# Optimization experiments

Measured on AMD Instinct MI355X. Metric: run time of the kernel, lower is better.

The kernel has to match this reference:

```python
import jax, jax.numpy as jnp
import numpy as np

A0 = 0.5291772105638411
KE = 14.399645351950548


def _softplus_inverse(x):
    return x + np.log(-np.expm1(-x))


def _sigma(x):
    # exp(-1/clamp(x,1e-12)) underflows to 0 for x<=0, so the where is nan-free
    return jnp.where(x > 0, jnp.exp(-1.0 / jnp.maximum(x, 1e-12)), 0.0)


def _switch(x, x_on, x_off):
    c = (x - x_on) / (x_off - x_on)
    s1 = _sigma(1.0 - c)
    s0 = _sigma(c)
    return s1 / (s1 + s0 + 1e-12)


def setup_inputs() -> dict:
    key = jax.random.key(0)
    k0, k1, k2, k3, k4 = jax.random.split(key, 5)
    N = 100000
    E = 6400000
    atomic_numbers = jax.random.uniform(k0, (N,), jnp.float32, 1.0, 30.0)
    cutoffs = jax.random.uniform(k1, (E, 1), jnp.float32)
    lengths = jax.random.uniform(k2, (E, 1), jnp.float32, 0.5, 3.0)
    senders = jax.random.randint(k3, (E,), 0, N)
    receivers = jax.random.randint(k4, (E,), 0, N)
    init = dict(a1=3.2, a2=0.9423, a3=0.4028, a4=0.2016,
                c1=0.1818, c2=0.5099, c3=0.2802, c4=0.02817,
                p=0.23, d=1.0 / (0.8854 * A0))
    params = {k + '_raw': jnp.asarray([_softplus_inverse(v)], jnp.float32)
              for k, v in init.items()}
    out = {'atomic_numbers': atomic_numbers, 'cutoffs': cutoffs,
           'senders': senders, 'receivers': receivers,
           'lengths': lengths, 'num_nodes': N}
    out.update(params)
    return out


def reference(atomic_numbers, cutoffs, senders, receivers, lengths, num_nodes,
              a1_raw, a2_raw, a3_raw, a4_raw,
              c1_raw, c2_raw, c3_raw, c4_raw, p_raw, d_raw):
    sp = jax.nn.softplus
    a1, a2, a3, a4 = sp(a1_raw), sp(a2_raw), sp(a3_raw), sp(a4_raw)
    c1, c2, c3, c4 = sp(c1_raw), sp(c2_raw), sp(c3_raw), sp(c4_raw)
    p, d = sp(p_raw), sp(d_raw)
    c_sum = c1 + c2 + c3 + c4
    c1, c2, c3, c4 = c1 / c_sum, c2 / c_sum, c3 / c_sum, c4 / c_sum

    cut = cutoffs[:, 0]   # [E]
    L = lengths[:, 0]     # [E]
    z_i = atomic_numbers[receivers]
    z_j = atomic_numbers[senders]

    x = KE * cut * (z_i * z_j) / jnp.maximum(L, 1e-6)
    rzd = L * (jnp.power(z_i, p) + jnp.power(z_j, p)) * d
    y = (c1 * jnp.exp(-a1 * rzd) + c2 * jnp.exp(-a2 * rzd)
         + c3 * jnp.exp(-a3 * rzd) + c4 * jnp.exp(-a4 * rzd))
    w = _switch(L, 0.0, 1.5)
    e_rep_edge = w * x * y * 0.5
    return jax.ops.segment_sum(e_rep_edge, receivers, num_segments=num_nodes)[:, None]
```

## Files before the change

kernel.cpp:

```cpp
#include <hip/hip_runtime.h>
#include <math.h>

#define C0KE 7.199822675975274f
#define LOG2E 1.4426950408889634f
#define BSHIFT 8
#define NB 391
#define NBP 392
#define K1B 512
#define K1T 1024
#define PLCAP 12512

__device__ __forceinline__ float softplusf(float x) {
    return (x > 20.0f) ? x : log1pf(__expf(x));
}

struct ZblParams { float A1, A2, A3, A4, c1, c2, c3, c4, p; };

__device__ __forceinline__ void load_params(
    const float* a1r, const float* a2r, const float* a3r, const float* a4r,
    const float* c1r, const float* c2r, const float* c3r, const float* c4r,
    const float* pr, const float* dr, ZblParams* P)
{
    float d  = softplusf(dr[0]);
    float s  = d * LOG2E;
    P->A1 = softplusf(a1r[0]) * s;
    P->A2 = softplusf(a2r[0]) * s;
    P->A3 = softplusf(a3r[0]) * s;
    P->A4 = softplusf(a4r[0]) * s;
    float c1 = softplusf(c1r[0]), c2 = softplusf(c2r[0]);
    float c3 = softplusf(c3r[0]), c4 = softplusf(c4r[0]);
    float inv = 1.0f / (c1 + c2 + c3 + c4);
    P->c1 = c1 * inv; P->c2 = c2 * inv; P->c3 = c3 * inv; P->c4 = c4 * inv;
    P->p = softplusf(pr[0]);
}

__device__ __forceinline__ float edge_energy_fast(
    float l, float cut_, float zi, float zj, const ZblParams& P)
{
    float c  = l * (1.0f / 1.5f);
    float om = 1.0f - c;
    float s1 = __builtin_amdgcn_exp2f(-LOG2E * __builtin_amdgcn_rcpf(om));
    float s0 = __builtin_amdgcn_exp2f(-LOG2E * __builtin_amdgcn_rcpf(c));
    float w  = s1 * __builtin_amdgcn_rcpf(s1 + s0);
    float x  = C0KE * cut_ * zi * zj * __builtin_amdgcn_rcpf(l);
    float S  = __builtin_amdgcn_exp2f(P.p * __builtin_amdgcn_logf(zi))
             + __builtin_amdgcn_exp2f(P.p * __builtin_amdgcn_logf(zj));
    float t  = l * S;
    float y  = P.c1 * __builtin_amdgcn_exp2f(-P.A1 * t)
             + P.c2 * __builtin_amdgcn_exp2f(-P.A2 * t)
             + P.c3 * __builtin_amdgcn_exp2f(-P.A3 * t)
             + P.c4 * __builtin_amdgcn_exp2f(-P.A4 * t);
    return w * x * y;
}

__global__ __launch_bounds__(K1T) void zbl_build(
    const float* __restrict__ z, const float* __restrict__ cut,
    const int* __restrict__ snd, const int* __restrict__ rcv,
    const float* __restrict__ len,
    const float* __restrict__ a1r, const float* __restrict__ a2r,
    const float* __restrict__ a3r, const float* __restrict__ a4r,
    const float* __restrict__ c1r, const float* __restrict__ c2r,
    const float* __restrict__ c3r, const float* __restrict__ c4r,
    const float* __restrict__ pr,  const float* __restrict__ dr,
    unsigned* __restrict__ T,
    unsigned* __restrict__ Pg,
    int RSTRIDE, int EPB, int E)
{
    __shared__ ZblParams P;
    __shared__ unsigned chist[NB];
    __shared__ unsigned cbase[NBP];
    __shared__ unsigned fillc[NB];
    __shared__ unsigned wavesum[16];
    __shared__ unsigned pl[PLCAP];

    const int tid = threadIdx.x;
    if (tid == 0)
        load_params(a1r, a2r, a3r, a4r, c1r, c2r, c3r, c4r, pr, dr, &P);
    for (int b = tid; b < NB; b += K1T) { chist[b] = 0u; fillc[b] = 0u; }
    __syncthreads();
    const ZblParams Pl = P;

    const int blk = blockIdx.x;
    const int e0 = blk * EPB;
    const int e1 = min(e0 + EPB, E);
    const int nv = (e1 > e0) ? ((e1 - e0) >> 2) : 0;
    const int qb = e0 >> 2;
    const int etail = e0 + (nv << 2);

    for (int q = tid; q < nv; q += K1T) {
        float4 l4 = ((const float4*)len)[qb + q];
        int4   r4 = ((const int4*)rcv)[qb + q];
        if (l4.x < 1.5f) atomicAdd(&chist[((unsigned)r4.x) >> BSHIFT], 1u);
        if (l4.y < 1.5f) atomicAdd(&chist[((unsigned)r4.y) >> BSHIFT], 1u);
        if (l4.z < 1.5f) atomicAdd(&chist[((unsigned)r4.z) >> BSHIFT], 1u);
        if (l4.w < 1.5f) atomicAdd(&chist[((unsigned)r4.w) >> BSHIFT], 1u);
    }
    for (int e = etail + tid; e < e1; e += K1T)
        if (len[e] < 1.5f) atomicAdd(&chist[((unsigned)rcv[e]) >> BSHIFT], 1u);
    __syncthreads();

    {
        const int lane = tid & 63, wv = tid >> 6;
        unsigned own = (tid < NB) ? chist[tid] : 0u;
        unsigned v = own;
        #pragma unroll
        for (int o = 1; o < 64; o <<= 1) {
            unsigned u = __shfl_up(v, o);
            if (lane >= o) v += u;
        }
        if (lane == 63 && wv < 7) wavesum[wv] = v;
        __syncthreads();
        if (wv == 0) {
            unsigned s = (lane < 7) ? wavesum[lane] : 0u;
            #pragma unroll
            for (int o = 1; o < 8; o <<= 1) {
                unsigned u = __shfl_up(s, o);
                if (lane >= o) s += u;
            }
            if (lane < 7) wavesum[lane] = s;
        }
        __syncthreads();
        unsigned off = (wv > 0 && wv < 8) ? wavesum[wv - 1] : 0u;
        if (tid < NB) cbase[tid] = off + v - own;
        if (tid == 0) cbase[NB] = wavesum[6];
    }
    __syncthreads();

    const unsigned blkbase = (unsigned)blk * (unsigned)RSTRIDE;
    const unsigned trow = (unsigned)blk * (unsigned)NBP;
    for (int b = tid; b <= NB; b += K1T)
        T[trow + b] = blkbase + cbase[b];

    for (int q = tid; q < nv; q += K1T) {
        float4 l4 = ((const float4*)len)[qb + q];
        if (l4.x < 1.5f || l4.y < 1.5f || l4.z < 1.5f || l4.w < 1.5f) {
            float4 c4 = ((const float4*)cut)[qb + q];
            int4   s4 = ((const int4*)snd)[qb + q];
            int4   r4 = ((const int4*)rcv)[qb + q];
            float Ls[4] = {l4.x, l4.y, l4.z, l4.w};
            float Cs[4] = {c4.x, c4.y, c4.z, c4.w};
            int   Ss[4] = {s4.x, s4.y, s4.z, s4.w};
            int   Rs[4] = {r4.x, r4.y, r4.z, r4.w};
            #pragma unroll
            for (int k = 0; k < 4; ++k) {
                if (Ls[k] < 1.5f) {
                    unsigned r = (unsigned)Rs[k];
                    float v = edge_energy_fast(Ls[k], Cs[k],
                                               z[r], z[(unsigned)Ss[k]], Pl);
                    unsigned bk = r >> BSHIFT;
                    unsigned tk = atomicAdd(&fillc[bk], 1u);
                    pl[cbase[bk] + tk] = (__float_as_uint(v) & 0xFFFFFF00u)
                                       | (r & 0xFFu);
                }
            }
        }
    }
    for (int e = etail + tid; e < e1; e += K1T) {
        float l = len[e];
        if (l < 1.5f) {
            unsigned r = (unsigned)rcv[e];
            float v = edge_energy_fast(l, cut[e], z[r], z[(unsigned)snd[e]], Pl);
            unsigned bk = r >> BSHIFT;
            unsigned tk = atomicAdd(&fillc[bk], 1u);
            pl[cbase[bk] + tk] = (__float_as_uint(v) & 0xFFFFFF00u) | (r & 0xFFu);
        }
    }
    __syncthreads();

    const unsigned csum = cbase[NB];
    for (unsigned s = tid; s < csum; s += K1T)
        Pg[blkbase + s] = pl[s];
}

__global__ __launch_bounds__(512) void zbl_reduce(
    const unsigned* __restrict__ T, const unsigned* __restrict__ Pg,
    float* __restrict__ out, int N)
{
    __shared__ float acc[256];
    const int tid = threadIdx.x;
    if (tid < 256) acc[tid] = 0.0f;
    __syncthreads();

    const int b = blockIdx.x;
    for (int r = tid; r < K1B; r += 512) {
        const unsigned* row = T + (size_t)r * NBP;
        unsigned s = row[b];
        unsigned e = row[b + 1];
        for (unsigned i = s; i < e; ++i) {
            unsigned p = Pg[i];
            atomicAdd(&acc[p & 255u], __uint_as_float(p & 0xFFFFFF00u));
        }
    }
    __syncthreads();

    int n = (b << BSHIFT) + tid;
    if (tid < 256 && n < N) out[n] = acc[tid];
}

__global__ __launch_bounds__(256) void zbl_direct(
    const float* __restrict__ z, const float* __restrict__ cut,
    const int* __restrict__ snd, const int* __restrict__ rcv,
    const float* __restrict__ len,
    const float* __restrict__ a1r, const float* __restrict__ a2r,
    const float* __restrict__ a3r, const float* __restrict__ a4r,
    const float* __restrict__ c1r, const float* __restrict__ c2r,
    const float* __restrict__ c3r, const float* __restrict__ c4r,
    const float* __restrict__ pr,  const float* __restrict__ dr,
    float* __restrict__ out, int n4, int E)
{
    __shared__ ZblParams P;
    if (threadIdx.x == 0)
        load_params(a1r, a2r, a3r, a4r, c1r, c2r, c3r, c4r, pr, dr, &P);
    __syncthreads();
    const ZblParams Pl = P;

    int i = blockIdx.x * blockDim.x + threadIdx.x;
    if (i >= n4) return;
    int base = i * 4;
    float cs[4], Ls[4]; int ss[4], rr[4]; int cnt;
    if (base + 4 <= E) {
        float4 c4v = ((const float4*)cut)[i];
        float4 l4v = ((const float4*)len)[i];
        int4   s4v = ((const int4*)snd)[i];
        int4   r4v = ((const int4*)rcv)[i];
        cs[0]=c4v.x; cs[1]=c4v.y; cs[2]=c4v.z; cs[3]=c4v.w;
        Ls[0]=l4v.x; Ls[1]=l4v.y; Ls[2]=l4v.z; Ls[3]=l4v.w;
        ss[0]=s4v.x; ss[1]=s4v.y; ss[2]=s4v.z; ss[3]=s4v.w;
        rr[0]=r4v.x; rr[1]=r4v.y; rr[2]=r4v.z; rr[3]=r4v.w;
        cnt = 4;
    } else {
        cnt = E - base;
        for (int k = 0; k < cnt; ++k) {
            cs[k] = cut[base+k]; Ls[k] = len[base+k];
            ss[k] = snd[base+k]; rr[k] = rcv[base+k];
        }
    }
    #pragma unroll
    for (int k = 0; k < 4; ++k) {
        if (k >= cnt) break;
        if (Ls[k] < 1.5f) {
            float e_rep = edge_energy_fast(Ls[k], cs[k], z[rr[k]], z[ss[k]], Pl);
            unsafeAtomicAdd(&out[rr[k]], e_rep);
        }
    }
}

extern "C" void kernel_launch(void* const* d_in, const int* in_sizes, int n_in,
                              void* d_out, int out_size, void* d_ws, size_t ws_size,
                              hipStream_t stream) {
    const float* z   = (const float*)d_in[0];
    const float* cut = (const float*)d_in[1];
    const int*   snd = (const int*)d_in[2];
    const int*   rcv = (const int*)d_in[3];
    const float* len = (const float*)d_in[4];
    const float* a1r = (const float*)d_in[6];
    const float* a2r = (const float*)d_in[7];
    const float* a3r = (const float*)d_in[8];
    const float* a4r = (const float*)d_in[9];
    const float* c1r = (const float*)d_in[10];
    const float* c2r = (const float*)d_in[11];
    const float* c3r = (const float*)d_in[12];
    const float* c4r = (const float*)d_in[13];
    const float* pr  = (const float*)d_in[14];
    const float* dr  = (const float*)d_in[15];

    float* out = (float*)d_out;
    int E = in_sizes[2];
    int N = out_size;

    int EPB = (((E + K1B - 1) / K1B) + 3) & ~3;
    int RSTRIDE = (EPB + 15) & ~15;
    size_t tsz = ((size_t)K1B * NBP * sizeof(unsigned) + 255) & ~(size_t)255;
    size_t need1 = tsz + (size_t)K1B * RSTRIDE * sizeof(unsigned);

    if (EPB <= PLCAP && ws_size >= need1) {
        unsigned* T  = (unsigned*)d_ws;
        unsigned* Pg = (unsigned*)((char*)d_ws + tsz);
        hipLaunchKernelGGL(zbl_build, dim3(K1B), dim3(K1T), 0, stream,
                           z, cut, snd, rcv, len,
                           a1r, a2r, a3r, a4r, c1r, c2r, c3r, c4r, pr, dr,
                           T, Pg, RSTRIDE, EPB, E);
        hipLaunchKernelGGL(zbl_reduce, dim3(NB), dim3(512), 0, stream,
                           (const unsigned*)T, (const unsigned*)Pg, out, N);
    } else {
        hipMemsetAsync(d_out, 0, (size_t)N * sizeof(float), stream);
        int n4 = (E + 3) / 4;
        int blocks = (n4 + 255) / 256;
        hipLaunchKernelGGL(zbl_direct, dim3(blocks), dim3(256), 0, stream,
                           z, cut, snd, rcv, len,
                           a1r, a2r, a3r, a4r, c1r, c2r, c3r, c4r, pr, dr,
                           out, n4, E);
    }
}
```

Baseline: 207.3 us.

## Replace counting-sort bucketing with fixed-slot per-bucket staging plus global-atomic overflow

The build kernel drops the histogram pass and prefix scan. Each block now writes edges into fixed 16-slot regions per receiver bucket in shared memory, and any overflow goes to global atomics on the output, which is zeroed by a memset first. The reduce kernel reads fixed-stride uint4 slot regions, skips sentinel entries, and adds its sums into the output. This removes a second pass over the len/rcv arrays, the scan and the offset table. The cost is more blocks with 512 threads, a larger padded staging buffer, and possible global atomic contention when a bucket exceeds its slots.

```diff
diff --git a/kernel.cpp b/kernel.cpp
--- a/kernel.cpp
+++ b/kernel.cpp
@@ -4,11 +4,12 @@
 #define C0KE 7.199822675975274f
 #define LOG2E 1.4426950408889634f
 #define BSHIFT 8
-#define NB 391
-#define NBP 392
-#define K1B 512
-#define K1T 1024
-#define PLCAP 12512
+#define NBK 391
+#define SLOTS 16
+#define REG (NBK * SLOTS)
+#define NBLK 1024
+#define K1T 512
+#define SENTINEL 0xFFFFFFFFu
 
 __device__ __forceinline__ float softplusf(float x) {
     return (x > 20.0f) ? x : log1pf(__expf(x));
@@ -62,21 +63,19 @@
     const float* __restrict__ c1r, const float* __restrict__ c2r,
     const float* __restrict__ c3r, const float* __restrict__ c4r,
     const float* __restrict__ pr,  const float* __restrict__ dr,
-    unsigned* __restrict__ T,
     unsigned* __restrict__ Pg,
-    int RSTRIDE, int EPB, int E)
+    float* __restrict__ out,
+    int EPB, int E)
 {
     __shared__ ZblParams P;
-    __shared__ unsigned chist[NB];
-    __shared__ unsigned cbase[NBP];
-    __shared__ unsigned fillc[NB];
-    __shared__ unsigned wavesum[16];
-    __shared__ unsigned pl[PLCAP];
+    __shared__ unsigned slots[REG];
+    __shared__ unsigned fillc[NBK];
 
     const int tid = threadIdx.x;
     if (tid == 0)
         load_params(a1r, a2r, a3r, a4r, c1r, c2r, c3r, c4r, pr, dr, &P);
-    for (int b = tid; b < NB; b += K1T) { chist[b] = 0u; fillc[b] = 0u; }
+    for (int i = tid; i < REG; i += K1T) slots[i] = SENTINEL;
+    for (int b = tid; b < NBK; b += K1T) fillc[b] = 0u;
     __syncthreads();
     const ZblParams Pl = P;
 
@@ -86,57 +85,17 @@
     const int nv = (e1 > e0) ? ((e1 - e0) >> 2) : 0;
     const int qb = e0 >> 2;
     const int etail = e0 + (nv << 2);
+    const float4* Lq = (const float4*)len;
+    const int4*   Rq = (const int4*)rcv;
+    const float4* Cq = (const float4*)cut;
+    const int4*   Sq = (const int4*)snd;
 
     for (int q = tid; q < nv; q += K1T) {
-        float4 l4 = ((const float4*)len)[qb + q];
-        int4   r4 = ((const int4*)rcv)[qb + q];
-        if (l4.x < 1.5f) atomicAdd(&chist[((unsigned)r4.x) >> BSHIFT], 1u);
-        if (l4.y < 1.5f) atomicAdd(&chist[((unsigned)r4.y) >> BSHIFT], 1u);
-        if (l4.z < 1.5f) atomicAdd(&chist[((unsigned)r4.z) >> BSHIFT], 1u);
-        if (l4.w < 1.5f) atomicAdd(&chist[((unsigned)r4.w) >> BSHIFT], 1u);
-    }
-    for (int e = etail + tid; e < e1; e += K1T)
-        if (len[e] < 1.5f) atomicAdd(&chist[((unsigned)rcv[e]) >> BSHIFT], 1u);
-    __syncthreads();
-
-    {
-        const int lane = tid & 63, wv = tid >> 6;
-        unsigned own = (tid < NB) ? chist[tid] : 0u;
-        unsigned v = own;
-        #pragma unroll
-        for (int o = 1; o < 64; o <<= 1) {
-            unsigned u = __shfl_up(v, o);
-            if (lane >= o) v += u;
-        }
-        if (lane == 63 && wv < 7) wavesum[wv] = v;
-        __syncthreads();
-        if (wv == 0) {
-            unsigned s = (lane < 7) ? wavesum[lane] : 0u;
-            #pragma unroll
-            for (int o = 1; o < 8; o <<= 1) {
-                unsigned u = __shfl_up(s, o);
-                if (lane >= o) s += u;
-            }
-            if (lane < 7) wavesum[lane] = s;
-        }
-        __syncthreads();
-        unsigned off = (wv > 0 && wv < 8) ? wavesum[wv - 1] : 0u;
-        if (tid < NB) cbase[tid] = off + v - own;
-        if (tid == 0) cbase[NB] = wavesum[6];
-    }
-    __syncthreads();
-
-    const unsigned blkbase = (unsigned)blk * (unsigned)RSTRIDE;
-    const unsigned trow = (unsigned)blk * (unsigned)NBP;
-    for (int b = tid; b <= NB; b += K1T)
-        T[trow + b] = blkbase + cbase[b];
-
-    for (int q = tid; q < nv; q += K1T) {
-        float4 l4 = ((const float4*)len)[qb + q];
+        float4 l4 = Lq[qb + q];
         if (l4.x < 1.5f || l4.y < 1.5f || l4.z < 1.5f || l4.w < 1.5f) {
-            float4 c4 = ((const float4*)cut)[qb + q];
-            int4   s4 = ((const int4*)snd)[qb + q];
-            int4   r4 = ((const int4*)rcv)[qb + q];
+            int4   r4 = Rq[qb + q];
+            float4 c4 = Cq[qb + q];
+            int4   s4 = Sq[qb + q];
             float Ls[4] = {l4.x, l4.y, l4.z, l4.w};
             float Cs[4] = {c4.x, c4.y, c4.z, c4.w};
             int   Ss[4] = {s4.x, s4.y, s4.z, s4.w};
@@ -146,11 +105,15 @@
                 if (Ls[k] < 1.5f) {
                     unsigned r = (unsigned)Rs[k];
                     float v = edge_energy_fast(Ls[k], Cs[k],
-                                               z[r], z[(unsigned)Ss[k]], Pl);
+                                z[r], z[(unsigned)Ss[k]], Pl);
                     unsigned bk = r >> BSHIFT;
                     unsigned tk = atomicAdd(&fillc[bk], 1u);
-                    pl[cbase[bk] + tk] = (__float_as_uint(v) & 0xFFFFFF00u)
-                                       | (r & 0xFFu);
+                    if (tk < SLOTS) {
+                        slots[bk * SLOTS + tk] =
+                            (__float_as_uint(v) & 0xFFFFFF00u) | (r & 0xFFu);
+                    } else {
+                        unsafeAtomicAdd(&out[r], v);
+                    }
                 }
             }
         }
@@ -162,19 +125,22 @@
             float v = edge_energy_fast(l, cut[e], z[r], z[(unsigned)snd[e]], Pl);
             unsigned bk = r >> BSHIFT;
             unsigned tk = atomicAdd(&fillc[bk], 1u);
-            pl[cbase[bk] + tk] = (__float_as_uint(v) & 0xFFFFFF00u) | (r & 0xFFu);
-        }
-    }
-    __syncthreads();
-
-    const unsigned csum = cbase[NB];
-    for (unsigned s = tid; s < csum; s += K1T)
-        Pg[blkbase + s] = pl[s];
+            if (tk < SLOTS)
+                slots[bk * SLOTS + tk] =
+                    (__float_as_uint(v) & 0xFFFFFF00u) | (r & 0xFFu);
+            else
+                unsafeAtomicAdd(&out[r], v);
+        }
+    }
+    __syncthreads();
+
+    unsigned base = (unsigned)blk * (unsigned)REG;
+    for (int i = tid; i < REG; i += K1T)
+        Pg[base + i] = slots[i];
 }
 
 __global__ __launch_bounds__(512) void zbl_reduce(
-    const unsigned* __restrict__ T, const unsigned* __restrict__ Pg,
-    float* __restrict__ out, int N)
+    const unsigned* __restrict__ Pg, float* __restrict__ out, int N)
 {
     __shared__ float acc[256];
     const int tid = threadIdx.x;
@@ -182,19 +148,25 @@
     __syncthreads();
 
     const int b = blockIdx.x;
-    for (int r = tid; r < K1B; r += 512) {
-        const unsigned* row = T + (size_t)r * NBP;
-        unsigned s = row[b];
-        unsigned e = row[b + 1];
-        for (unsigned i = s; i < e; ++i) {
-            unsigned p = Pg[i];
-            atomicAdd(&acc[p & 255u], __uint_as_float(p & 0xFFFFFF00u));
-        }
+    const uint4* Pq = (const uint4*)Pg;
+    const int total = NBLK * (SLOTS / 4);
+    for (int lin = tid; lin < total; lin += 512) {
+        int r = lin >> 2, q = lin & 3;
+        uint4 u = Pq[(size_t)r * (REG / 4) + (size_t)b * (SLOTS / 4) + q];
+        if (u.x != SENTINEL)
+            atomicAdd(&acc[u.x & 255u], __uint_as_float(u.x & 0xFFFFFF00u));
+        if (u.y != SENTINEL)
+            atomicAdd(&acc[u.y & 255u], __uint_as_float(u.y & 0xFFFFFF00u));
+        if (u.z != SENTINEL)
+            atomicAdd(&acc[u.z & 255u], __uint_as_float(u.z & 0xFFFFFF00u));
+        if (u.w != SENTINEL)
+            atomicAdd(&acc[u.w & 255u], __uint_as_float(u.w & 0xFFFFFF00u));
     }
     __syncthreads();
 
     int n = (b << BSHIFT) + tid;
-    if (tid < 256 && n < N) out[n] = acc[tid];
+    if (tid < 256 && n < N)
+        out[n] += acc[tid];
 }
 
 __global__ __launch_bounds__(256) void zbl_direct(
@@ -268,22 +240,20 @@
     int E = in_sizes[2];
     int N = out_size;
 
-    int EPB = (((E + K1B - 1) / K1B) + 3) & ~3;
-    int RSTRIDE = (EPB + 15) & ~15;
-    size_t tsz = ((size_t)K1B * NBP * sizeof(unsigned) + 255) & ~(size_t)255;
-    size_t need1 = tsz + (size_t)K1B * RSTRIDE * sizeof(unsigned);
-
-    if (EPB <= PLCAP && ws_size >= need1) {
-        unsigned* T  = (unsigned*)d_ws;
-        unsigned* Pg = (unsigned*)((char*)d_ws + tsz);
-        hipLaunchKernelGGL(zbl_build, dim3(K1B), dim3(K1T), 0, stream,
+    size_t need1 = (size_t)NBLK * REG * sizeof(unsigned);
+
+    hipMemsetAsync(d_out, 0, (size_t)N * sizeof(float), stream);
+
+    if (ws_size >= need1) {
+        int EPB = (((E + NBLK - 1) / NBLK) + 3) & ~3;
+        unsigned* Pg = (unsigned*)d_ws;
+        hipLaunchKernelGGL(zbl_build, dim3(NBLK), dim3(K1T), 0, stream,
                            z, cut, snd, rcv, len,
                            a1r, a2r, a3r, a4r, c1r, c2r, c3r, c4r, pr, dr,
-                           T, Pg, RSTRIDE, EPB, E);
-        hipLaunchKernelGGL(zbl_reduce, dim3(NB), dim3(512), 0, stream,
-                           (const unsigned*)T, (const unsigned*)Pg, out, N);
+                           Pg, out, EPB, E);
+        hipLaunchKernelGGL(zbl_reduce, dim3(NBK), dim3(512), 0, stream,
+                           (const unsigned*)Pg, out, N);
     } else {
-        hipMemsetAsync(d_out, 0, (size_t)N * sizeof(float), stream);
         int n4 = (E + 3) / 4;
         int blocks = (n4 + 255) / 256;
         hipLaunchKernelGGL(zbl_direct, dim3(blocks), dim3(256), 0, stream,
```

New measurement: 205.4 us. About the same (-0.9%).
